# Optimization experiments

Measured on AMD Instinct MI355X. Metric: run time of the kernel, lower is better.

The kernel has to match this reference:

```python
import jax, jax.numpy as jnp
import numpy as np

KNOTS = 16
BOUND = 5.0
BATCH = 500000
X_DIM = 6          # split into lower(3) / upper(3)
C_DIM = 4
HID = 128
SPLINE_DIM = 3 * KNOTS - 1   # 47 (non-periodic)
LOWER = X_DIM // 2
OUT_DIM = LOWER * SPLINE_DIM


def setup_inputs() -> dict:
    key = jax.random.key(0)
    ks = jax.random.split(key, 10)
    def glorot(k, shape):
        fan_in, fan_out = shape
        s = jnp.sqrt(2.0 / (fan_in + fan_out))
        return (jax.random.normal(k, shape, jnp.float32) * s)
    return {
        "x": jax.random.normal(ks[0], (BATCH, X_DIM), jnp.float32),
        "c": jax.random.normal(ks[1], (BATCH, C_DIM), jnp.float32),
        "W1": glorot(ks[2], (LOWER + C_DIM + 0 + (X_DIM - LOWER), HID))[: X_DIM - LOWER + C_DIM],
        "b1": jnp.zeros((HID,), jnp.float32),
        "W2": glorot(ks[3], (HID, HID)),
        "b2": jnp.zeros((HID,), jnp.float32),
        "W3": glorot(ks[4], (HID, OUT_DIM)),
        "b3": jnp.zeros((OUT_DIM,), jnp.float32),
        "train": False,
    }


def _mlp(h, W1, b1, W2, b2, W3, b3):
    h = jax.nn.relu(h @ W1 + b1)
    h = jax.nn.relu(h @ W2 + b2)
    return h @ W3 + b3


def _rqs_forward(x, W, H, D, B):
    """Rational-quadratic spline (Durkan et al.) forward.
    x: [N,d]; W,H: [N,d,K] bin widths/heights; D: [N,d,K-1] interior derivs."""
    K = W.shape[-1]
    pad = jnp.full(W.shape[:-1] + (1,), -B, W.dtype)
    xk = jnp.concatenate([pad, -B + jnp.cumsum(W, axis=-1)], axis=-1)  # [N,d,K+1]
    yk = jnp.concatenate([pad, -B + jnp.cumsum(H, axis=-1)], axis=-1)
    one = jnp.ones(D.shape[:-1] + (1,), D.dtype)
    dk = jnp.concatenate([one, D, one], axis=-1)                        # [N,d,K+1]

    oob = (x <= -B) | (x >= B)
    xm = jnp.where(oob, -B, x)
    # bin index per element (searchsorted via comparison-sum)
    idx = jnp.clip(jnp.sum((xm[..., None] >= xk), axis=-1) - 1, 0, K - 1)[..., None]

    gat = lambda a, i: jnp.take_along_axis(a, i, axis=-1)[..., 0]
    xk_b = gat(xk, idx)
    yk_b = gat(yk, idx)
    wk = gat(xk, idx + 1) - xk_b
    hk = gat(yk, idx + 1) - yk_b
    dk_b = gat(dk, idx)
    dk1 = gat(dk, idx + 1)

    sk = hk / wk
    relx = jnp.clip((xm - xk_b) / wk, 0.0, 1.0)
    r1 = relx * (1.0 - relx)
    den = sk + (dk1 + dk_b - 2.0 * sk) * r1
    num = hk * (sk * relx * relx + dk_b * r1)
    y = yk_b + num / den
    ld = (2.0 * jnp.log(sk)
          + jnp.log(dk1 * relx * relx + 2.0 * sk * r1 + dk_b * (1.0 - relx) ** 2)
          - 2.0 * jnp.log(den))

    y = jnp.where(oob, x, y)
    ld = jnp.where(oob, 0.0, ld)
    return y, jnp.sum(ld, axis=1)


def reference(x, c, W1, b1, W2, b2, W3, b3, train):
    lower, upper = x[:, :LOWER], x[:, LOWER:]
    h = jnp.hstack((upper, c))
    p = _mlp(h, W1, b1, W2, b2, W3, b3)
    p = p.reshape(-1, LOWER, SPLINE_DIM)
    Wb, Hb, Db = jnp.split(p, [KNOTS, 2 * KNOTS], axis=2)
    Wb = 2.0 * BOUND * jax.nn.softmax(Wb, axis=-1)
    Hb = 2.0 * BOUND * jax.nn.softmax(Hb, axis=-1)
    Db = jax.nn.softplus(Db)
    lo_t, log_det = _rqs_forward(lower, Wb, Hb, Db, BOUND)
    y = jnp.hstack((lo_t, upper))
    return y, log_det
```

## Files before the change

### kernel.cpp

```cpp
#include <hip/hip_runtime.h>
#include <math.h>


#define TILE 128
#define NT   256
#define HID  128
#define OUTD 141
#define INS  40
#define HS   136
#define PRS  48
#define SRS  152
#define BND  5.0f
#define T1   0.5413248546f

typedef __bf16 bf16;
typedef _Float16 f16;
typedef __attribute__((ext_vector_type(8))) __bf16 bf16x8;
typedef __attribute__((ext_vector_type(8))) _Float16 f16x8;
typedef __attribute__((ext_vector_type(4))) float f32x4;

#define W1P_ELEMS (8 * 64 * 8)
#define W2P_ELEMS (8 * 4 * 64 * 8)
#define W3P_ELEMS (9 * 4 * 64 * 8)

#define SMEM_BYTES 46592

__global__ void nsc_prepack(const float* __restrict__ W1, const float* __restrict__ W2,
                            const float* __restrict__ W3,
                            bf16* __restrict__ W1p, bf16* __restrict__ W2p,
                            bf16* __restrict__ W3p) {
    int f = blockIdx.x * 256 + threadIdx.x;
    int lane = f & 63, lm = lane & 15, lq = lane >> 4;
    if (f < 512) {
        int t = f >> 6;
        int n = t * 16 + lm;
        bf16x8 pk;
        #pragma unroll
        for (int j = 0; j < 8; ++j) {
            int k = lq * 8 + j;
            pk[j] = (k < 7) ? (bf16)W1[k * HID + n] : (bf16)0.f;
        }
        *(bf16x8*)&W1p[(size_t)f * 8] = pk;
    } else if (f < 512 + 2048) {
        int g2 = f - 512;
        int tk = g2 >> 6, t = tk >> 2, ks = tk & 3;
        int n = t * 16 + lm;
        bf16x8 pk;
        #pragma unroll
        for (int j = 0; j < 8; ++j) {
            int p = ks * 32 + lq * 8 + j;
            int k = ((p & 7) << 4) | (p >> 3);
            pk[j] = (bf16)W2[k * HID + n];
        }
        *(bf16x8*)&W2p[(size_t)g2 * 8] = pk;
    } else if (f < 512 + 2048 + 2304) {
        int g3 = f - 2560;
        int tk = g3 >> 6, t = tk >> 2, ks = tk & 3;
        int col = t * 16 + lm;
        bf16x8 pk;
        #pragma unroll
        for (int j = 0; j < 8; ++j) {
            int p = ks * 32 + lq * 8 + j;
            int k = ((p & 7) << 4) | (p >> 3);
            pk[j] = (col < OUTD) ? (bf16)W3[k * OUTD + col] : (bf16)0.f;
        }
        *(bf16x8*)&W3p[(size_t)g3 * 8] = pk;
    }
}

__global__ __launch_bounds__(NT, 3) void nsc_main(
    const float* __restrict__ x, const float* __restrict__ c,
    const bf16* __restrict__ W1p, const float* __restrict__ b1,
    const bf16* __restrict__ W2p, const float* __restrict__ b2,
    const bf16* __restrict__ W3p, const float* __restrict__ b3,
    float* __restrict__ out_y, float* __restrict__ out_ld, int N)
{
    __shared__ __align__(16) char smem[SMEM_BYTES];
    bf16*  shIn  = (bf16*)smem;
    bf16*  hbuf  = (bf16*)(smem + 10240);
    f16*   shp16 = (f16*)smem;
    float* shld  = (float*)(smem + 45056);

    const int tid  = threadIdx.x;
    const int g0   = blockIdx.x * TILE;
    const int lane = tid & 63;
    const int wv   = tid >> 6;
    const int lm   = lane & 15;
    const int lq   = lane >> 4;
    const int sbase = wv * 32;
    const int arow0 = sbase + lm;
    const int arow1 = sbase + 16 + lm;

    if (lane < 32) {
        int s = sbase + lane;
        int g = g0 + s;
        float v[7];
        if (g < N) {
            v[0] = x[g * 6 + 3]; v[1] = x[g * 6 + 4]; v[2] = x[g * 6 + 5];
            v[3] = c[g * 4];     v[4] = c[g * 4 + 1];
            v[5] = c[g * 4 + 2]; v[6] = c[g * 4 + 3];
        } else {
            #pragma unroll
            for (int k = 0; k < 7; ++k) v[k] = 0.f;
        }
        bf16x8 r0 = (bf16x8){(bf16)v[0], (bf16)v[1], (bf16)v[2], (bf16)v[3],
                             (bf16)v[4], (bf16)v[5], (bf16)v[6], (bf16)0.f};
        bf16x8 z  = (bf16x8){(bf16)0.f, (bf16)0.f, (bf16)0.f, (bf16)0.f,
                             (bf16)0.f, (bf16)0.f, (bf16)0.f, (bf16)0.f};
        *(bf16x8*)&shIn[s * INS]      = r0;
        *(bf16x8*)&shIn[s * INS + 8]  = z;
        *(bf16x8*)&shIn[s * INS + 16] = z;
        *(bf16x8*)&shIn[s * INS + 24] = z;
    }

    {
        f32x4 acc1[2][8];
        #pragma unroll
        for (int t = 0; t < 8; ++t) {
            float b = b1[t * 16 + lm];
            acc1[0][t] = (f32x4){b, b, b, b};
            acc1[1][t] = (f32x4){b, b, b, b};
        }
        bf16x8 a0 = *(const bf16x8*)&shIn[arow0 * INS + lq * 8];
        bf16x8 a1 = *(const bf16x8*)&shIn[arow1 * INS + lq * 8];
        #pragma unroll
        for (int t = 0; t < 8; ++t) {
            bf16x8 bf = *(const bf16x8*)&W1p[(size_t)(t * 64 + lane) * 8];
            acc1[0][t] = __builtin_amdgcn_mfma_f32_16x16x32_bf16(a0, bf, acc1[0][t], 0, 0, 0);
            acc1[1][t] = __builtin_amdgcn_mfma_f32_16x16x32_bf16(a1, bf, acc1[1][t], 0, 0, 0);
        }
        #pragma unroll
        for (int ar = 0; ar < 2; ++ar)
            #pragma unroll
            for (int r = 0; r < 4; ++r) {
                bf16x8 pk;
                #pragma unroll
                for (int t = 0; t < 8; ++t) pk[t] = (bf16)fmaxf(acc1[ar][t][r], 0.f);
                int s = sbase + ar * 16 + lq * 4 + r;
                *(bf16x8*)&hbuf[s * HS + lm * 8] = pk;
            }
    }

    {
        f32x4 acc2[2][8];
        #pragma unroll
        for (int t = 0; t < 8; ++t) {
            float b = b2[t * 16 + lm];
            acc2[0][t] = (f32x4){b, b, b, b};
            acc2[1][t] = (f32x4){b, b, b, b};
        }
        #pragma unroll
        for (int ks = 0; ks < 4; ++ks) {
            bf16x8 a0 = *(const bf16x8*)&hbuf[arow0 * HS + ks * 32 + lq * 8];
            bf16x8 a1 = *(const bf16x8*)&hbuf[arow1 * HS + ks * 32 + lq * 8];
            #pragma unroll
            for (int t = 0; t < 8; ++t) {
                bf16x8 bf = *(const bf16x8*)&W2p[(size_t)((t * 4 + ks) * 64 + lane) * 8];
                acc2[0][t] = __builtin_amdgcn_mfma_f32_16x16x32_bf16(a0, bf, acc2[0][t], 0, 0, 0);
                acc2[1][t] = __builtin_amdgcn_mfma_f32_16x16x32_bf16(a1, bf, acc2[1][t], 0, 0, 0);
            }
        }
        #pragma unroll
        for (int ar = 0; ar < 2; ++ar)
            #pragma unroll
            for (int r = 0; r < 4; ++r) {
                bf16x8 pk;
                #pragma unroll
                for (int t = 0; t < 8; ++t) pk[t] = (bf16)fmaxf(acc2[ar][t][r], 0.f);
                int s = sbase + ar * 16 + lq * 4 + r;
                *(bf16x8*)&hbuf[s * HS + lm * 8] = pk;
            }
    }

    f32x4 acc3[2][9];
    {
        #pragma unroll
        for (int t = 0; t < 9; ++t) {
            int col = t * 16 + lm;
            float b = (col < OUTD) ? b3[col] : 0.f;
            acc3[0][t] = (f32x4){b, b, b, b};
            acc3[1][t] = (f32x4){b, b, b, b};
        }
        #pragma unroll
        for (int ks = 0; ks < 4; ++ks) {
            bf16x8 a0 = *(const bf16x8*)&hbuf[arow0 * HS + ks * 32 + lq * 8];
            bf16x8 a1 = *(const bf16x8*)&hbuf[arow1 * HS + ks * 32 + lq * 8];
            #pragma unroll
            for (int t = 0; t < 9; ++t) {
                bf16x8 bf = *(const bf16x8*)&W3p[(size_t)((t * 4 + ks) * 64 + lane) * 8];
                acc3[0][t] = __builtin_amdgcn_mfma_f32_16x16x32_bf16(a0, bf, acc3[0][t], 0, 0, 0);
                acc3[1][t] = __builtin_amdgcn_mfma_f32_16x16x32_bf16(a1, bf, acc3[1][t], 0, 0, 0);
            }
        }
    }
    __syncthreads();

    #pragma unroll
    for (int t = 0; t < 9; ++t) {
        int col = t * 16 + lm;
        if (col < OUTD) {
            int d = (col >= 94) ? 2 : ((col >= 47) ? 1 : 0);
            int i = col - d * 47;
            #pragma unroll
            for (int ar = 0; ar < 2; ++ar)
                #pragma unroll
                for (int r = 0; r < 4; ++r) {
                    int s = sbase + ar * 16 + lq * 4 + r;
                    shp16[s * SRS + d * PRS + i] = (f16)acc3[ar][t][r];
                }
        }
    }
    __syncthreads();

    for (int pidx = tid; pidx < TILE * 3; pidx += NT) {
        const int s = pidx / 3, d = pidx - s * 3;
        const int g = g0 + s;
        if (g < N) {
            const f16* pr = &shp16[s * SRS + d * PRS];
            f16x8 v0 = *(const f16x8*)&pr[0];
            f16x8 v1 = *(const f16x8*)&pr[8];
            f16x8 v2 = *(const f16x8*)&pr[16];
            f16x8 v3 = *(const f16x8*)&pr[24];
            f16x8 v4 = *(const f16x8*)&pr[32];
            f16x8 v5 = *(const f16x8*)&pr[40];
            float wv_[16], hv[16], dl[15];
            #pragma unroll
            for (int i = 0; i < 8; ++i) {
                wv_[i] = (float)v0[i]; wv_[8 + i] = (float)v1[i];
                hv[i]  = (float)v2[i]; hv[8 + i]  = (float)v3[i];
            }
            #pragma unroll
            for (int i = 0; i < 8; ++i) dl[i] = (float)v4[i];
            #pragma unroll
            for (int i = 0; i < 7; ++i) dl[8 + i] = (float)v5[i];

            float sw = 0.f, sh = 0.f;
            #pragma unroll
            for (int i = 0; i < 16; ++i) { wv_[i] = __expf(wv_[i]); sw += wv_[i]; }
            #pragma unroll
            for (int i = 0; i < 16; ++i) { hv[i]  = __expf(hv[i]);  sh += hv[i]; }
            float cwn = 10.f * __builtin_amdgcn_rcpf(sw);
            float chn = 10.f * __builtin_amdgcn_rcpf(sh);
            #pragma unroll
            for (int i = 0; i < 16; ++i) { wv_[i] *= cwn; hv[i] *= chn; }

            float xv = x[g * 6 + d];
            bool oob = (xv <= -BND) || (xv >= BND);
            float xm = oob ? -BND : xv;

            float cumx = -BND + wv_[0], cumy = -BND + hv[0];
            float xk_b = -BND, yk_b = -BND;
            float wk = wv_[0], hk = hv[0];
            float d0l = T1, d1l = dl[0];
            #pragma unroll
            for (int i = 1; i < 16; ++i) {
                bool ge = (xm >= cumx);
                if (ge) {
                    xk_b = cumx; yk_b = cumy;
                    wk = wv_[i]; hk = hv[i];
                    d0l = dl[i - 1];
                    d1l = (i < 15) ? dl[i] : T1;
                }
                cumx += wv_[i]; cumy += hv[i];
            }
            float d0 = (d0l > 15.f) ? d0l : __logf(1.f + __expf(d0l));
            float d1 = (d1l > 15.f) ? d1l : __logf(1.f + __expf(d1l));

            float rwk = __builtin_amdgcn_rcpf(wk);
            float sk = hk * rwk;
            float relx = (xm - xk_b) * rwk;
            relx = fminf(fmaxf(relx, 0.f), 1.f);
            float r1 = relx * (1.f - relx);
            float den = sk + (d1 + d0 - 2.f * sk) * r1;
            float iden = __builtin_amdgcn_rcpf(den);
            float num = hk * (sk * relx * relx + d0 * r1);
            float y = yk_b + num * iden;
            float omr = 1.f - relx;
            float arg = d1 * relx * relx + 2.f * sk * r1 + d0 * omr * omr;
            float ratio = sk * iden;
            float ld = __logf(ratio * ratio * arg);
            if (oob) { y = xv; ld = 0.f; }

            out_y[g * 6 + d] = y;
            out_y[g * 6 + 3 + d] = x[g * 6 + 3 + d];
            shld[s * 3 + d] = ld;
        }
    }
    __syncthreads();

    if (tid < TILE) {
        int g = g0 + tid;
        if (g < N)
            out_ld[g] = shld[tid * 3] + shld[tid * 3 + 1] + shld[tid * 3 + 2];
    }
}

extern "C" void kernel_launch(void* const* d_in, const int* in_sizes, int n_in,
                              void* d_out, int out_size, void* d_ws, size_t ws_size,
                              hipStream_t stream) {
    const float* x  = (const float*)d_in[0];
    const float* c  = (const float*)d_in[1];
    const float* W1 = (const float*)d_in[2];
    const float* b1 = (const float*)d_in[3];
    const float* W2 = (const float*)d_in[4];
    const float* b2 = (const float*)d_in[5];
    const float* W3 = (const float*)d_in[6];
    const float* b3 = (const float*)d_in[7];

    const int N = in_sizes[0] / 6;
    float* out_y  = (float*)d_out;
    float* out_ld = (float*)d_out + (size_t)N * 6;

    bf16* W1p = (bf16*)d_ws;
    bf16* W2p = W1p + W1P_ELEMS;
    bf16* W3p = W2p + W2P_ELEMS;

    int nfrag = 512 + 2048 + 2304;
    nsc_prepack<<<(nfrag + 255) / 256, 256, 0, stream>>>(W1, W2, W3, W1p, W2p, W3p);

    int nblocks = (N + TILE - 1) / TILE;
    nsc_main<<<nblocks, NT, 0, stream>>>(x, c, W1p, b1, W2p, b2, W3p, b3,
                                         out_y, out_ld, N);
}
```

Before: 159.4 us.

## Halve block to two waves, hold weight fragments in registers across row blocks

```diff
diff --git a/kernel.cpp b/kernel.cpp
--- a/kernel.cpp
+++ b/kernel.cpp
@@ -3,10 +3,9 @@
 
 
 #define TILE 128
-#define NT   256
+#define NT   128
 #define HID  128
 #define OUTD 141
-#define INS  40
 #define HS   136
 #define PRS  48
 #define SRS  152
@@ -17,13 +16,14 @@
 typedef _Float16 f16;
 typedef __attribute__((ext_vector_type(8))) __bf16 bf16x8;
 typedef __attribute__((ext_vector_type(8))) _Float16 f16x8;
+typedef __attribute__((ext_vector_type(2))) _Float16 f16x2;
 typedef __attribute__((ext_vector_type(4))) float f32x4;
 
 #define W1P_ELEMS (8 * 64 * 8)
 #define W2P_ELEMS (8 * 4 * 64 * 8)
 #define W3P_ELEMS (9 * 4 * 64 * 8)
 
-#define SMEM_BYTES 46592
+#define SMEM_BYTES 40448
 
 __global__ void nsc_prepack(const float* __restrict__ W1, const float* __restrict__ W2,
                             const float* __restrict__ W3,
@@ -68,7 +68,7 @@
     }
 }
 
-__global__ __launch_bounds__(NT, 3) void nsc_main(
+__global__ __launch_bounds__(NT, 2) void nsc_main(
     const float* __restrict__ x, const float* __restrict__ c,
     const bf16* __restrict__ W1p, const float* __restrict__ b1,
     const bf16* __restrict__ W2p, const float* __restrict__ b2,
@@ -76,10 +76,9 @@
     float* __restrict__ out_y, float* __restrict__ out_ld, int N)
 {
     __shared__ __align__(16) char smem[SMEM_BYTES];
-    bf16*  shIn  = (bf16*)smem;
-    bf16*  hbuf  = (bf16*)(smem + 10240);
+    bf16*  hbuf  = (bf16*)smem;
     f16*   shp16 = (f16*)smem;
-    float* shld  = (float*)(smem + 45056);
+    float* shld  = (float*)(smem + 38912);
 
     const int tid  = threadIdx.x;
     const int g0   = blockIdx.x * TILE;
@@ -87,11 +86,9 @@
     const int wv   = tid >> 6;
     const int lm   = lane & 15;
     const int lq   = lane >> 4;
-    const int sbase = wv * 32;
-    const int arow0 = sbase + lm;
-    const int arow1 = sbase + 16 + lm;
-
-    if (lane < 32) {
+    const int sbase = wv * 64;
+
+    {
         int s = sbase + lane;
         int g = g0 + s;
         float v[7];
@@ -107,107 +104,131 @@
                              (bf16)v[4], (bf16)v[5], (bf16)v[6], (bf16)0.f};
         bf16x8 z  = (bf16x8){(bf16)0.f, (bf16)0.f, (bf16)0.f, (bf16)0.f,
                              (bf16)0.f, (bf16)0.f, (bf16)0.f, (bf16)0.f};
-        *(bf16x8*)&shIn[s * INS]      = r0;
-        *(bf16x8*)&shIn[s * INS + 8]  = z;
-        *(bf16x8*)&shIn[s * INS + 16] = z;
-        *(bf16x8*)&shIn[s * INS + 24] = z;
-    }
-
-    {
-        f32x4 acc1[2][8];
-        #pragma unroll
-        for (int t = 0; t < 8; ++t) {
-            float b = b1[t * 16 + lm];
-            acc1[0][t] = (f32x4){b, b, b, b};
-            acc1[1][t] = (f32x4){b, b, b, b};
-        }
-        bf16x8 a0 = *(const bf16x8*)&shIn[arow0 * INS + lq * 8];
-        bf16x8 a1 = *(const bf16x8*)&shIn[arow1 * INS + lq * 8];
-        #pragma unroll
-        for (int t = 0; t < 8; ++t) {
-            bf16x8 bf = *(const bf16x8*)&W1p[(size_t)(t * 64 + lane) * 8];
-            acc1[0][t] = __builtin_amdgcn_mfma_f32_16x16x32_bf16(a0, bf, acc1[0][t], 0, 0, 0);
-            acc1[1][t] = __builtin_amdgcn_mfma_f32_16x16x32_bf16(a1, bf, acc1[1][t], 0, 0, 0);
-        }
-        #pragma unroll
-        for (int ar = 0; ar < 2; ++ar)
+        *(bf16x8*)&hbuf[s * HS]      = r0;
+        *(bf16x8*)&hbuf[s * HS + 8]  = z;
+        *(bf16x8*)&hbuf[s * HS + 16] = z;
+        *(bf16x8*)&hbuf[s * HS + 24] = z;
+    }
+
+    float bb1[8], bb2[8], bb3[9];
+    #pragma unroll
+    for (int t = 0; t < 8; ++t) { bb1[t] = b1[t * 16 + lm]; bb2[t] = b2[t * 16 + lm]; }
+    #pragma unroll
+    for (int t = 0; t < 9; ++t) {
+        int col = t * 16 + lm;
+        bb3[t] = (col < OUTD) ? b3[col] : 0.f;
+    }
+
+    {
+        bf16x8 B1[8];
+        #pragma unroll
+        for (int t = 0; t < 8; ++t)
+            B1[t] = *(const bf16x8*)&W1p[(size_t)(t * 64 + lane) * 8];
+        #pragma unroll
+        for (int rb = 0; rb < 4; ++rb) {
+            const int rB = sbase + rb * 16;
+            bf16x8 a = *(const bf16x8*)&hbuf[(rB + lm) * HS + lq * 8];
+            f32x4 acc[8];
+            #pragma unroll
+            for (int t = 0; t < 8; ++t)
+                acc[t] = (f32x4){bb1[t], bb1[t], bb1[t], bb1[t]};
+            #pragma unroll
+            for (int t = 0; t < 8; ++t)
+                acc[t] = __builtin_amdgcn_mfma_f32_16x16x32_bf16(a, B1[t], acc[t], 0, 0, 0);
             #pragma unroll
             for (int r = 0; r < 4; ++r) {
                 bf16x8 pk;
                 #pragma unroll
-                for (int t = 0; t < 8; ++t) pk[t] = (bf16)fmaxf(acc1[ar][t][r], 0.f);
-                int s = sbase + ar * 16 + lq * 4 + r;
-                *(bf16x8*)&hbuf[s * HS + lm * 8] = pk;
-            }
-    }
-
-    {
-        f32x4 acc2[2][8];
-        #pragma unroll
-        for (int t = 0; t < 8; ++t) {
-            float b = b2[t * 16 + lm];
-            acc2[0][t] = (f32x4){b, b, b, b};
-            acc2[1][t] = (f32x4){b, b, b, b};
-        }
-        #pragma unroll
-        for (int ks = 0; ks < 4; ++ks) {
-            bf16x8 a0 = *(const bf16x8*)&hbuf[arow0 * HS + ks * 32 + lq * 8];
-            bf16x8 a1 = *(const bf16x8*)&hbuf[arow1 * HS + ks * 32 + lq * 8];
-            #pragma unroll
-            for (int t = 0; t < 8; ++t) {
-                bf16x8 bf = *(const bf16x8*)&W2p[(size_t)((t * 4 + ks) * 64 + lane) * 8];
-                acc2[0][t] = __builtin_amdgcn_mfma_f32_16x16x32_bf16(a0, bf, acc2[0][t], 0, 0, 0);
-                acc2[1][t] = __builtin_amdgcn_mfma_f32_16x16x32_bf16(a1, bf, acc2[1][t], 0, 0, 0);
-            }
-        }
-        #pragma unroll
-        for (int ar = 0; ar < 2; ++ar)
+                for (int t = 0; t < 8; ++t) pk[t] = (bf16)fmaxf(acc[t][r], 0.f);
+                *(bf16x8*)&hbuf[(rB + lq * 4 + r) * HS + lm * 8] = pk;
+            }
+        }
+    }
+
+    {
+        bf16x8 B2[32];
+        #pragma unroll
+        for (int i = 0; i < 32; ++i)
+            B2[i] = *(const bf16x8*)&W2p[(size_t)(i * 64 + lane) * 8];
+        #pragma unroll
+        for (int rb = 0; rb < 4; ++rb) {
+            const int rB = sbase + rb * 16;
+            bf16x8 a[4];
+            #pragma unroll
+            for (int ks = 0; ks < 4; ++ks)
+                a[ks] = *(const bf16x8*)&hbuf[(rB + lm) * HS + ks * 32 + lq * 8];
+            f32x4 acc[8];
+            #pragma unroll
+            for (int t = 0; t < 8; ++t)
+                acc[t] = (f32x4){bb2[t], bb2[t], bb2[t], bb2[t]};
+            #pragma unroll
+            for (int ks = 0; ks < 4; ++ks)
+                #pragma unroll
+                for (int t = 0; t < 8; ++t)
+                    acc[t] = __builtin_amdgcn_mfma_f32_16x16x32_bf16(a[ks], B2[t * 4 + ks], acc[t], 0, 0, 0);
             #pragma unroll
             for (int r = 0; r < 4; ++r) {
                 bf16x8 pk;
                 #pragma unroll
-                for (int t = 0; t < 8; ++t) pk[t] = (bf16)fmaxf(acc2[ar][t][r], 0.f);
-                int s = sbase + ar * 16 + lq * 4 + r;
-                *(bf16x8*)&hbuf[s * HS + lm * 8] = pk;
-            }
-    }
-
-    f32x4 acc3[2][9];
-    {
+                for (int t = 0; t < 8; ++t) pk[t] = (bf16)fmaxf(acc[t][r], 0.f);
+                *(bf16x8*)&hbuf[(rB + lq * 4 + r) * HS + lm * 8] = pk;
+            }
+        }
+    }
+
+    f16x2 stash[4][9][2];
+    {
+        bf16x8 B3[36];
+        #pragma unroll
+        for (int i = 0; i < 36; ++i)
+            B3[i] = *(const bf16x8*)&W3p[(size_t)(i * 64 + lane) * 8];
+        #pragma unroll
+        for (int rb = 0; rb < 4; ++rb) {
+            const int rB = sbase + rb * 16;
+            bf16x8 a[4];
+            #pragma unroll
+            for (int ks = 0; ks < 4; ++ks)
+                a[ks] = *(const bf16x8*)&hbuf[(rB + lm) * HS + ks * 32 + lq * 8];
+            f32x4 acc[9];
+            #pragma unroll
+            for (int t = 0; t < 9; ++t)
+                acc[t] = (f32x4){bb3[t], bb3[t], bb3[t], bb3[t]};
+            #pragma unroll
+            for (int ks = 0; ks < 4; ++ks)
+                #pragma unroll
+                for (int t = 0; t < 9; ++t)
+                    acc[t] = __builtin_amdgcn_mfma_f32_16x16x32_bf16(a[ks], B3[t * 4 + ks], acc[t], 0, 0, 0);
+            #pragma unroll
+            for (int t = 0; t < 9; ++t) {
+                stash[rb][t][0] = (f16x2){(f16)acc[t][0], (f16)acc[t][1]};
+                stash[rb][t][1] = (f16x2){(f16)acc[t][2], (f16)acc[t][3]};
+            }
+        }
+    }
+    __syncthreads();
+
+    {
+        int off3[9]; bool val3[9];
         #pragma unroll
         for (int t = 0; t < 9; ++t) {
             int col = t * 16 + lm;
-            float b = (col < OUTD) ? b3[col] : 0.f;
-            acc3[0][t] = (f32x4){b, b, b, b};
-            acc3[1][t] = (f32x4){b, b, b, b};
-        }
-        #pragma unroll
-        for (int ks = 0; ks < 4; ++ks) {
-            bf16x8 a0 = *(const bf16x8*)&hbuf[arow0 * HS + ks * 32 + lq * 8];
-            bf16x8 a1 = *(const bf16x8*)&hbuf[arow1 * HS + ks * 32 + lq * 8];
+            val3[t] = (col < OUTD);
+            int d = (col >= 94) ? 2 : ((col >= 47) ? 1 : 0);
+            off3[t] = d * PRS + (col - d * 47);
+        }
+        #pragma unroll
+        for (int rb = 0; rb < 4; ++rb) {
+            const int rB = sbase + rb * 16;
             #pragma unroll
             for (int t = 0; t < 9; ++t) {
-                bf16x8 bf = *(const bf16x8*)&W3p[(size_t)((t * 4 + ks) * 64 + lane) * 8];
-                acc3[0][t] = __builtin_amdgcn_mfma_f32_16x16x32_bf16(a0, bf, acc3[0][t], 0, 0, 0);
-                acc3[1][t] = __builtin_amdgcn_mfma_f32_16x16x32_bf16(a1, bf, acc3[1][t], 0, 0, 0);
-            }
-        }
-    }
-    __syncthreads();
-
-    #pragma unroll
-    for (int t = 0; t < 9; ++t) {
-        int col = t * 16 + lm;
-        if (col < OUTD) {
-            int d = (col >= 94) ? 2 : ((col >= 47) ? 1 : 0);
-            int i = col - d * 47;
-            #pragma unroll
-            for (int ar = 0; ar < 2; ++ar)
-                #pragma unroll
-                for (int r = 0; r < 4; ++r) {
-                    int s = sbase + ar * 16 + lq * 4 + r;
-                    shp16[s * SRS + d * PRS + i] = (f16)acc3[ar][t][r];
+                if (val3[t]) {
+                    #pragma unroll
+                    for (int r = 0; r < 4; ++r) {
+                        int s = rB + lq * 4 + r;
+                        shp16[s * SRS + off3[t]] = stash[rb][t][r >> 1][r & 1];
+                    }
                 }
+            }
         }
     }
     __syncthreads();
@@ -288,7 +309,7 @@
     }
     __syncthreads();
 
-    if (tid < TILE) {
+    {
         int g = g0 + tid;
         if (g < N)
             out_ld[g] = shld[tid * 3] + shld[tid * 3 + 1] + shld[tid * 3 + 2];
```

After: 170.2 us. 6.8% more time.
